# Kernel optimization log

Hardware: AMD Instinct MI355X
Metric: run time of the kernel (lower is better)

## Reference

```python
import jax, jax.numpy as jnp
import numpy as np

U, I, H, E = 50000, 50000, 128, 800000


def segment_softmax(vals, seg, num):
    m = jax.ops.segment_max(vals, seg, num_segments=num)
    ex = jnp.exp(vals - m[seg])
    s = jax.ops.segment_sum(ex, seg, num_segments=num)
    return ex / s[seg]


def setup_inputs() -> dict:
    key = jax.random.key(0)
    ks = jax.random.split(key, 16)
    scale = 1.0 / np.sqrt(H)
    inp = {
        "u_emb": jax.random.normal(ks[0], (U, H), jnp.float32),
        "i_emb": jax.random.normal(ks[1], (I, H), jnp.float32),
        "pVui": jax.random.normal(ks[2], (E, H), jnp.float32),
        "pKiu": jax.random.normal(ks[3], (E, H), jnp.float32),
        "w1": jax.random.normal(ks[4], (H, H), jnp.float32) * scale,
        "w2": jax.random.normal(ks[5], (H, H), jnp.float32) * scale,
        "w1b": jax.random.normal(ks[6], (H, H), jnp.float32) * scale,
        "w2b": jax.random.normal(ks[7], (H, H), jnp.float32) * scale,
        "w3": jax.random.normal(ks[8], (H, H), jnp.float32) * scale,
        "w4": jax.random.normal(ks[9], (H, H), jnp.float32) * scale,
        "edge_index": jax.random.randint(ks[10], (2, E), 0, min(U, I), jnp.int64),
        "last_u": jax.random.randint(ks[11], (2, U), 0, I, jnp.int64),
        "last_i": jax.random.randint(ks[12], (2, I), 0, U, jnp.int64),
        "graph": jnp.zeros((1,), jnp.int64),
    }
    return inp


def reference(u_emb, i_emb, pVui, pKiu, w1, w2, w1b, w2b, w3, w4,
              edge_index, last_u, last_i, graph):
    sqrt_d = np.sqrt(float(u_emb.shape[1])).astype if False else float(np.sqrt(u_emb.shape[1]))
    nu, ni = u_emb.shape[0], i_emb.shape[0]
    src_u, dst_i = edge_index[0], edge_index[1]  # per-edge (user, item)

    # ---- longterm ----
    um_att = u_emb @ w2.T            # [U,H]
    im_att = i_emb @ w1.T            # [I,H]
    # sparse_dense_mul(edge_index, um_att @ im_att.T) -> per-edge dot products
    e_vals = jnp.sum(um_att[src_u] * im_att[dst_i], axis=-1)  # [E]
    e_ui = e_vals + jnp.sum(um_att[src_u] * pVui, axis=-1)
    alphas = segment_softmax(e_ui / sqrt_d, src_u, nu)        # softmax over items per user
    e_iu = e_vals + jnp.sum(im_att[dst_i] * pKiu, axis=-1)
    betas = segment_softmax(e_iu / sqrt_d, dst_i, ni)         # softmax over users per item
    um_b = u_emb @ w2b.T
    im_b = i_emb @ w1b.T
    hLu = jax.ops.segment_sum(alphas[:, None] * (im_b[dst_i] + pKiu), src_u, num_segments=nu)
    hLi = jax.ops.segment_sum(betas[:, None] * (um_b[src_u] + pVui), dst_i, num_segments=ni)

    # ---- shortterm ----
    last_item = i_emb[last_u[1]] @ w3.T   # [U,H] last item embedding per user
    last_user = u_emb[last_i[1]] @ w4.T   # [I,H] last user embedding per item
    a_vals = jnp.sum(last_item[src_u] * im_att[dst_i], axis=-1)
    s_alphas = segment_softmax(a_vals / sqrt_d, src_u, nu)
    b_vals = jnp.sum(last_user[src_u] * im_att[dst_i], axis=-1)
    s_betas = segment_softmax(b_vals / sqrt_d, dst_i, ni)
    # pass_messages with p = ones -> messages + 1
    hSu = jax.ops.segment_sum(s_alphas[:, None] * (im_att[dst_i] + 1.0), src_u, num_segments=nu)
    hSi = jax.ops.segment_sum(s_betas[:, None] * (um_att[src_u] + 1.0), dst_i, num_segments=ni)
    return (hLu, hSu, hLi, hSi)
```

## Files before the change

### kernel.cpp

```cpp
#include <hip/hip_runtime.h>
#include <hip/hip_bf16.h>
#include <math.h>


#define WB 1024

typedef float fvec4 __attribute__((ext_vector_type(4)));

__device__ __forceinline__ float4 nt_load4(const float* p) {
    fvec4 v = __builtin_nontemporal_load((const fvec4*)p);
    return make_float4(v.x, v.y, v.z, v.w);
}
__device__ __forceinline__ float dot4(float4 a, float4 b) {
    return a.x * b.x + a.y * b.y + a.z * b.z + a.w * b.w;
}

struct Gemm6Desc {
    const float* X[6];
    const float* W[6];
    float*       O[6];
    const int*   g[6];
    int          ostride[6];
    int          nrows[6];
};

__global__ __launch_bounds__(256) void gemm6_kernel(Gemm6Desc d)
{
    __shared__ float Xl[64 * 32];
    __shared__ float Wl[128 * 32];
    const int j6 = blockIdx.y;
    const float* __restrict__ X = d.X[j6];
    const float* __restrict__ W = d.W[j6];
    float* __restrict__ O       = d.O[j6];
    const int* __restrict__ gidx = d.g[j6];
    const int ostride = d.ostride[j6];
    const int nrows   = d.nrows[j6];

    const int t  = threadIdx.x;
    const int tx = t & 15;
    const int ty = t >> 4;
    const int brow = blockIdx.x * 64;
    if (brow >= nrows) return;

    float acc[4][8];
#pragma unroll
    for (int j = 0; j < 4; ++j)
#pragma unroll
        for (int i = 0; i < 8; ++i) acc[j][i] = 0.f;

    for (int k0 = 0; k0 < 128; k0 += 32) {
        __syncthreads();
#pragma unroll
        for (int u = 0; u < 2; ++u) {
            int idx4 = t + u * 256;
            int r  = idx4 >> 3;
            int k4 = idx4 & 7;
            int row = brow + r;
            float4 v = make_float4(0.f, 0.f, 0.f, 0.f);
            if (row < nrows) {
                int g = gidx ? gidx[row] : row;
                v = *(const float4*)(X + (size_t)g * 128 + k0 + k4 * 4);
            }
            int sw = k4 ^ ((r >> 3) & 7);
            *(float4*)(Xl + r * 32 + sw * 4) = v;
        }
#pragma unroll
        for (int u = 0; u < 4; ++u) {
            int idx4 = t + u * 256;
            int c  = idx4 >> 3;
            int k4 = idx4 & 7;
            float4 v = *(const float4*)(W + (size_t)c * 128 + k0 + k4 * 4);
            int sw = k4 ^ ((c >> 3) & 7);
            *(float4*)(Wl + c * 32 + sw * 4) = v;
        }
        __syncthreads();
#pragma unroll
        for (int k4 = 0; k4 < 8; ++k4) {
            float4 xv[4], wv[8];
#pragma unroll
            for (int j = 0; j < 4; ++j) {
                int r = ty * 4 + j;
                xv[j] = *(const float4*)(Xl + r * 32 + ((k4 ^ ((r >> 3) & 7)) * 4));
            }
#pragma unroll
            for (int i = 0; i < 8; ++i) {
                int c = tx * 8 + i;
                wv[i] = *(const float4*)(Wl + c * 32 + ((k4 ^ ((c >> 3) & 7)) * 4));
            }
#pragma unroll
            for (int j = 0; j < 4; ++j)
#pragma unroll
                for (int i = 0; i < 8; ++i) {
                    acc[j][i] += xv[j].x * wv[i].x;
                    acc[j][i] += xv[j].y * wv[i].y;
                    acc[j][i] += xv[j].z * wv[i].z;
                    acc[j][i] += xv[j].w * wv[i].w;
                }
        }
    }
#pragma unroll
    for (int j = 0; j < 4; ++j) {
        int row = brow + ty * 4 + j;
        if (row < nrows) {
            float* op = O + (size_t)row * ostride + tx * 8;
            *(float4*)(op)     = make_float4(acc[j][0], acc[j][1], acc[j][2], acc[j][3]);
            *(float4*)(op + 4) = make_float4(acc[j][4], acc[j][5], acc[j][6], acc[j][7]);
        }
    }
}

__global__ __launch_bounds__(256) void hist_kernel(
    const int* __restrict__ ei, int E,
    int* __restrict__ deg_u, int* __restrict__ deg_i)
{
    int e = blockIdx.x * 256 + threadIdx.x;
    if (e < E) {
        atomicAdd(&deg_u[ei[e]], 1);
        atomicAdd(&deg_i[ei[E + e]], 1);
    }
}

__global__ __launch_bounds__(256) void scan_blocksums_kernel(
    const int* __restrict__ deg_u, int nu, int nbu,
    const int* __restrict__ deg_i, int ni,
    int* __restrict__ bsum)
{
    int b = blockIdx.x;
    const int* deg; int n; int base;
    if (b < nbu) { deg = deg_u; n = nu; base = b * WB; }
    else         { deg = deg_i; n = ni; base = (b - nbu) * WB; }
    int t = threadIdx.x;
    int s = 0;
#pragma unroll
    for (int j = 0; j < 4; ++j) {
        int i = base + t * 4 + j;
        if (i < n) s += deg[i];
    }
#pragma unroll
    for (int o = 32; o > 0; o >>= 1) s += __shfl_xor(s, o);
    __shared__ int wt[4];
    if ((t & 63) == 0) wt[t >> 6] = s;
    __syncthreads();
    if (t == 0) bsum[b] = wt[0] + wt[1] + wt[2] + wt[3];
}

__global__ void scan_partials_kernel(
    const int* __restrict__ bsum, int* __restrict__ bscan,
    int nbu, int nbi,
    int* __restrict__ off_u, int nu, int* __restrict__ off_i, int ni)
{
    if (threadIdx.x != 0) return;
    if (blockIdx.x == 0) {
        int c = 0;
        for (int b = 0; b < nbu; ++b) { bscan[b] = c; c += bsum[b]; }
        off_u[nu] = c;
    } else {
        int c = 0;
        for (int b = 0; b < nbi; ++b) { bscan[nbu + b] = c; c += bsum[nbu + b]; }
        off_i[ni] = c;
    }
}

__global__ __launch_bounds__(256) void scan_final_kernel(
    const int* __restrict__ deg_u, int nu, int nbu,
    const int* __restrict__ deg_i, int ni,
    const int* __restrict__ bscan,
    int* __restrict__ off_u, int* __restrict__ cur_u,
    int* __restrict__ off_i, int* __restrict__ cur_i)
{
    int b = blockIdx.x;
    const int* deg; int n; int base; int* off; int* cur;
    if (b < nbu) { deg = deg_u; n = nu; base = b * WB; off = off_u; cur = cur_u; }
    else         { deg = deg_i; n = ni; base = (b - nbu) * WB; off = off_i; cur = cur_i; }
    int t = threadIdx.x;
    int lane = t & 63, w = t >> 6;
    int v[4];
    int s = 0;
#pragma unroll
    for (int j = 0; j < 4; ++j) {
        int i = base + t * 4 + j;
        v[j] = (i < n) ? deg[i] : 0;
        s += v[j];
    }
    int inc = s;
#pragma unroll
    for (int o = 1; o < 64; o <<= 1) {
        int x = __shfl_up(inc, o);
        if (lane >= o) inc += x;
    }
    int excl = inc - s;
    __shared__ int wt[4];
    if (lane == 63) wt[w] = inc;
    __syncthreads();
    int wbase = 0;
    for (int j = 0; j < w; ++j) wbase += wt[j];
    int e = bscan[b] + wbase + excl;
#pragma unroll
    for (int j = 0; j < 4; ++j) {
        int i = base + t * 4 + j;
        if (i < n) { off[i] = e; cur[i] = e; }
        e += v[j];
    }
}

__global__ __launch_bounds__(256) void scatter_ids_kernel(
    const int* __restrict__ ei, int E,
    int* __restrict__ cur_u, int* __restrict__ cur_i,
    int2* __restrict__ eu_list, int2* __restrict__ ei_list)
{
    int e = blockIdx.x * 256 + threadIdx.x;
    if (e < E) {
        int u = ei[e], v = ei[E + e];
        int pu = atomicAdd(&cur_u[u], 1);
        eu_list[pu] = make_int2(v, e);
        int pi = atomicAdd(&cur_i[v], 1);
        ei_list[pi] = make_int2(u, e);
    }
}

__global__ __launch_bounds__(256) void gather_u_kernel(
    const float* __restrict__ fusedU,
    const float* __restrict__ fusedI,
    const float* __restrict__ last_item, const float* __restrict__ last_user,
    const float* __restrict__ pVui, const float* __restrict__ pKiu,
    const int2* __restrict__ lst,
    const int* __restrict__ off_u,
    float2* __restrict__ x24,
    float* __restrict__ hLu, float* __restrict__ hSu, int U, float inv_sqrt_d)
{
    const int wid  = (int)(((size_t)blockIdx.x * blockDim.x + threadIdx.x) >> 6);
    const int lane = threadIdx.x & 63;
    if (wid >= U) return;
    const int g = lane >> 4;
    const int q = lane & 15;

    const float4* fu4 = (const float4*)(fusedU    + (size_t)wid * 256);
    const float4* li4 = (const float4*)(last_item + (size_t)wid * 128);
    const float4* lu4 = (const float4*)(last_user + (size_t)wid * 128);
    const float4 um0 = fu4[q],      um1 = fu4[q + 16];
    const float4 li0 = li4[q],      li1 = li4[q + 16];
    const float4 lu0 = lu4[q],      lu1 = lu4[q + 16];

    float4 a1l = make_float4(0.f,0.f,0.f,0.f), a1h = make_float4(0.f,0.f,0.f,0.f);
    float4 a3l = make_float4(0.f,0.f,0.f,0.f), a3h = make_float4(0.f,0.f,0.f,0.f);
    float s1 = 0.f, s3 = 0.f;
    const int e0 = off_u[wid], e1 = off_u[wid + 1];

    int eA = e0 + g, eB = eA + 4;
    bool vA = eA < e1, vB = eB < e1;
    int2 rA = vA ? lst[eA] : make_int2(0, 0);
    int2 rB = vB ? lst[eB] : rA;

    while (vA) {
        int eA2 = eA + 8, eB2 = eB + 8;
        bool vA2 = eA2 < e1, vB2 = eB2 < e1;
        int2 rA2 = vA2 ? lst[eA2] : make_int2(0, 0);
        int2 rB2 = vB2 ? lst[eB2] : rA2;

        const float4* fIA = (const float4*)(fusedI + (size_t)rA.x * 256);
        const float*  pvA = pVui + (size_t)rA.y * 128;
        const float*  pkA = pKiu + (size_t)rA.y * 128;
        const float4* fIB = (const float4*)(fusedI + (size_t)rB.x * 256);
        const float*  pvB = pVui + (size_t)rB.y * 128;
        const float*  pkB = pKiu + (size_t)rB.y * 128;

        float4 iaA0 = fIA[q],      iaA1 = fIA[q + 16];
        float4 ibA0 = fIA[32 + q], ibA1 = fIA[48 + q];
        float4 pvA0 = nt_load4(pvA + q * 4), pvA1 = nt_load4(pvA + 64 + q * 4);
        float4 pkA0 = nt_load4(pkA + q * 4), pkA1 = nt_load4(pkA + 64 + q * 4);
        float4 iaB0 = fIB[q],      iaB1 = fIB[q + 16];
        float4 ibB0 = fIB[32 + q], ibB1 = fIB[48 + q];
        float4 pvB0 = nt_load4(pvB + q * 4), pvB1 = nt_load4(pvB + 64 + q * 4);
        float4 pkB0 = nt_load4(pkB + q * 4), pkB1 = nt_load4(pkB + 64 + q * 4);

        float pA0 = dot4(um0, iaA0) + dot4(um1, iaA1);
        float qA1 = pA0 + dot4(um0, pvA0) + dot4(um1, pvA1);
        float qA2 = pA0 + dot4(iaA0, pkA0) + dot4(iaA1, pkA1);
        float qA3 = dot4(li0, iaA0) + dot4(li1, iaA1);
        float qA4 = dot4(lu0, iaA0) + dot4(lu1, iaA1);
        float pB0 = dot4(um0, iaB0) + dot4(um1, iaB1);
        float qB1 = pB0 + dot4(um0, pvB0) + dot4(um1, pvB1);
        float qB2 = pB0 + dot4(iaB0, pkB0) + dot4(iaB1, pkB1);
        float qB3 = dot4(li0, iaB0) + dot4(li1, iaB1);
        float qB4 = dot4(lu0, iaB0) + dot4(lu1, iaB1);
#pragma unroll
        for (int o = 8; o > 0; o >>= 1) {
            qA1 += __shfl_xor(qA1, o); qA2 += __shfl_xor(qA2, o);
            qA3 += __shfl_xor(qA3, o); qA4 += __shfl_xor(qA4, o);
            qB1 += __shfl_xor(qB1, o); qB2 += __shfl_xor(qB2, o);
            qB3 += __shfl_xor(qB3, o); qB4 += __shfl_xor(qB4, o);
        }
        float x1A = __expf(qA1 * inv_sqrt_d);
        float x2A = __expf(qA2 * inv_sqrt_d);
        float x3A = __expf(qA3 * inv_sqrt_d);
        float x4A = __expf(qA4 * inv_sqrt_d);
        float mB  = vB ? 1.f : 0.f;
        float x1B = __expf(qB1 * inv_sqrt_d) * mB;
        float x2B = __expf(qB2 * inv_sqrt_d);
        float x3B = __expf(qB3 * inv_sqrt_d) * mB;
        float x4B = __expf(qB4 * inv_sqrt_d);

        a1l.x += x1A*(ibA0.x+pkA0.x) + x1B*(ibB0.x+pkB0.x);
        a1l.y += x1A*(ibA0.y+pkA0.y) + x1B*(ibB0.y+pkB0.y);
        a1l.z += x1A*(ibA0.z+pkA0.z) + x1B*(ibB0.z+pkB0.z);
        a1l.w += x1A*(ibA0.w+pkA0.w) + x1B*(ibB0.w+pkB0.w);
        a1h.x += x1A*(ibA1.x+pkA1.x) + x1B*(ibB1.x+pkB1.x);
        a1h.y += x1A*(ibA1.y+pkA1.y) + x1B*(ibB1.y+pkB1.y);
        a1h.z += x1A*(ibA1.z+pkA1.z) + x1B*(ibB1.z+pkB1.z);
        a1h.w += x1A*(ibA1.w+pkA1.w) + x1B*(ibB1.w+pkB1.w);
        a3l.x += x3A*(iaA0.x+1.f) + x3B*(iaB0.x+1.f);
        a3l.y += x3A*(iaA0.y+1.f) + x3B*(iaB0.y+1.f);
        a3l.z += x3A*(iaA0.z+1.f) + x3B*(iaB0.z+1.f);
        a3l.w += x3A*(iaA0.w+1.f) + x3B*(iaB0.w+1.f);
        a3h.x += x3A*(iaA1.x+1.f) + x3B*(iaB1.x+1.f);
        a3h.y += x3A*(iaA1.y+1.f) + x3B*(iaB1.y+1.f);
        a3h.z += x3A*(iaA1.z+1.f) + x3B*(iaB1.z+1.f);
        a3h.w += x3A*(iaA1.w+1.f) + x3B*(iaB1.w+1.f);
        s1 += x1A + x1B; s3 += x3A + x3B;
        if (q == 0) {
            x24[rA.y] = make_float2(x2A, x4A);
            if (vB) x24[rB.y] = make_float2(x2B, x4B);
        }
        eA = eA2; eB = eB2; vA = vA2; vB = vB2; rA = rA2; rB = rB2;
    }
#pragma unroll
    for (int o = 16; o <= 32; o <<= 1) {
        a1l.x += __shfl_xor(a1l.x, o); a1l.y += __shfl_xor(a1l.y, o);
        a1l.z += __shfl_xor(a1l.z, o); a1l.w += __shfl_xor(a1l.w, o);
        a1h.x += __shfl_xor(a1h.x, o); a1h.y += __shfl_xor(a1h.y, o);
        a1h.z += __shfl_xor(a1h.z, o); a1h.w += __shfl_xor(a1h.w, o);
        a3l.x += __shfl_xor(a3l.x, o); a3l.y += __shfl_xor(a3l.y, o);
        a3l.z += __shfl_xor(a3l.z, o); a3l.w += __shfl_xor(a3l.w, o);
        a3h.x += __shfl_xor(a3h.x, o); a3h.y += __shfl_xor(a3h.y, o);
        a3h.z += __shfl_xor(a3h.z, o); a3h.w += __shfl_xor(a3h.w, o);
        s1 += __shfl_xor(s1, o);       s3 += __shfl_xor(s3, o);
    }
    if (lane < 16) {
        float r1 = (s1 > 0.f) ? 1.f / s1 : 0.f;
        float r3 = (s3 > 0.f) ? 1.f / s3 : 0.f;
        float4* oL = (float4*)(hLu + (size_t)wid * 128);
        float4* oS = (float4*)(hSu + (size_t)wid * 128);
        oL[q]      = make_float4(a1l.x*r1, a1l.y*r1, a1l.z*r1, a1l.w*r1);
        oL[q + 16] = make_float4(a1h.x*r1, a1h.y*r1, a1h.z*r1, a1h.w*r1);
        oS[q]      = make_float4(a3l.x*r3, a3l.y*r3, a3l.z*r3, a3l.w*r3);
        oS[q + 16] = make_float4(a3h.x*r3, a3h.y*r3, a3h.z*r3, a3h.w*r3);
    }
}

__global__ __launch_bounds__(256) void gather_i_kernel(
    const float* __restrict__ fusedU,
    const float* __restrict__ pVui,
    const int2* __restrict__ lst,
    const int* __restrict__ off_i,
    const float2* __restrict__ x24,
    float* __restrict__ hLi, float* __restrict__ hSi, int I)
{
    const int wid  = (int)(((size_t)blockIdx.x * blockDim.x + threadIdx.x) >> 6);
    const int lane = threadIdx.x & 63;
    if (wid >= I) return;
    const int g = lane >> 4;
    const int q = lane & 15;

    float4 a2l = make_float4(0.f,0.f,0.f,0.f), a2h = make_float4(0.f,0.f,0.f,0.f);
    float4 a4l = make_float4(0.f,0.f,0.f,0.f), a4h = make_float4(0.f,0.f,0.f,0.f);
    float s2 = 0.f, s4 = 0.f;
    const int e0 = off_i[wid], e1 = off_i[wid + 1];

    int eA = e0 + g, eB = eA + 4;
    bool vA = eA < e1, vB = eB < e1;
    int2 rA = vA ? lst[eA] : make_int2(0, 0);
    int2 rB = vB ? lst[eB] : rA;

    while (vA) {
        int eA2 = eA + 8, eB2 = eB + 8;
        bool vA2 = eA2 < e1, vB2 = eB2 < e1;
        int2 rA2 = vA2 ? lst[eA2] : make_int2(0, 0);
        int2 rB2 = vB2 ? lst[eB2] : rA2;

        const float4* fUA = (const float4*)(fusedU + (size_t)rA.x * 256);
        const float*  pvA = pVui + (size_t)rA.y * 128;
        const float4* fUB = (const float4*)(fusedU + (size_t)rB.x * 256);
        const float*  pvB = pVui + (size_t)rB.y * 128;

        float2 xA = x24[rA.y];
        float2 xB = x24[rB.y];
        float4 uaA0 = fUA[q],      uaA1 = fUA[q + 16];
        float4 ubA0 = fUA[32 + q], ubA1 = fUA[48 + q];
        float4 pvA0 = nt_load4(pvA + q * 4), pvA1 = nt_load4(pvA + 64 + q * 4);
        float4 uaB0 = fUB[q],      uaB1 = fUB[q + 16];
        float4 ubB0 = fUB[32 + q], ubB1 = fUB[48 + q];
        float4 pvB0 = nt_load4(pvB + q * 4), pvB1 = nt_load4(pvB + 64 + q * 4);

        if (!vB) { xB.x = 0.f; xB.y = 0.f; }
        a2l.x += xA.x*(ubA0.x+pvA0.x) + xB.x*(ubB0.x+pvB0.x);
        a2l.y += xA.x*(ubA0.y+pvA0.y) + xB.x*(ubB0.y+pvB0.y);
        a2l.z += xA.x*(ubA0.z+pvA0.z) + xB.x*(ubB0.z+pvB0.z);
        a2l.w += xA.x*(ubA0.w+pvA0.w) + xB.x*(ubB0.w+pvB0.w);
        a2h.x += xA.x*(ubA1.x+pvA1.x) + xB.x*(ubB1.x+pvB1.x);
        a2h.y += xA.x*(ubA1.y+pvA1.y) + xB.x*(ubB1.y+pvB1.y);
        a2h.z += xA.x*(ubA1.z+pvA1.z) + xB.x*(ubB1.z+pvB1.z);
        a2h.w += xA.x*(ubA1.w+pvA1.w) + xB.x*(ubB1.w+pvB1.w);
        a4l.x += xA.y*(uaA0.x+1.f) + xB.y*(uaB0.x+1.f);
        a4l.y += xA.y*(uaA0.y+1.f) + xB.y*(uaB0.y+1.f);
        a4l.z += xA.y*(uaA0.z+1.f) + xB.y*(uaB0.z+1.f);
        a4l.w += xA.y*(uaA0.w+1.f) + xB.y*(uaB0.w+1.f);
        a4h.x += xA.y*(uaA1.x+1.f) + xB.y*(uaB1.x+1.f);
        a4h.y += xA.y*(uaA1.y+1.f) + xB.y*(uaB1.y+1.f);
        a4h.z += xA.y*(uaA1.z+1.f) + xB.y*(uaB1.z+1.f);
        a4h.w += xA.y*(uaA1.w+1.f) + xB.y*(uaB1.w+1.f);
        s2 += xA.x + xB.x; s4 += xA.y + xB.y;

        eA = eA2; eB = eB2; vA = vA2; vB = vB2; rA = rA2; rB = rB2;
    }
#pragma unroll
    for (int o = 16; o <= 32; o <<= 1) {
        a2l.x += __shfl_xor(a2l.x, o); a2l.y += __shfl_xor(a2l.y, o);
        a2l.z += __shfl_xor(a2l.z, o); a2l.w += __shfl_xor(a2l.w, o);
        a2h.x += __shfl_xor(a2h.x, o); a2h.y += __shfl_xor(a2h.y, o);
        a2h.z += __shfl_xor(a2h.z, o); a2h.w += __shfl_xor(a2h.w, o);
        a4l.x += __shfl_xor(a4l.x, o); a4l.y += __shfl_xor(a4l.y, o);
        a4l.z += __shfl_xor(a4l.z, o); a4l.w += __shfl_xor(a4l.w, o);
        a4h.x += __shfl_xor(a4h.x, o); a4h.y += __shfl_xor(a4h.y, o);
        a4h.z += __shfl_xor(a4h.w - a4h.w + a4h.z, o); a4h.w += __shfl_xor(a4h.w, o);
        s2 += __shfl_xor(s2, o);       s4 += __shfl_xor(s4, o);
    }
    if (lane < 16) {
        float r2 = (s2 > 0.f) ? 1.f / s2 : 0.f;
        float r4 = (s4 > 0.f) ? 1.f / s4 : 0.f;
        float4* oL = (float4*)(hLi + (size_t)wid * 128);
        float4* oS = (float4*)(hSi + (size_t)wid * 128);
        oL[q]      = make_float4(a2l.x*r2, a2l.y*r2, a2l.z*r2, a2l.w*r2);
        oL[q + 16] = make_float4(a2h.x*r2, a2h.y*r2, a2h.z*r2, a2h.w*r2);
        oS[q]      = make_float4(a4l.x*r4, a4l.y*r4, a4l.z*r4, a4l.w*r4);
        oS[q + 16] = make_float4(a4h.x*r4, a4h.y*r4, a4h.z*r4, a4h.w*r4);
    }
}

extern "C" void kernel_launch(void* const* d_in, const int* in_sizes, int n_in,
                              void* d_out, int out_size, void* d_ws, size_t ws_size,
                              hipStream_t stream)
{
    const float* u_emb = (const float*)d_in[0];
    const float* i_emb = (const float*)d_in[1];
    const float* pVui  = (const float*)d_in[2];
    const float* pKiu  = (const float*)d_in[3];
    const float* w1    = (const float*)d_in[4];
    const float* w2    = (const float*)d_in[5];
    const float* w1b   = (const float*)d_in[6];
    const float* w2b   = (const float*)d_in[7];
    const float* w3    = (const float*)d_in[8];
    const float* w4    = (const float*)d_in[9];
    const int* edge_index = (const int*)d_in[10];
    const int* last_u     = (const int*)d_in[11];
    const int* last_i     = (const int*)d_in[12];

    const int U = in_sizes[0] / 128;
    const int I = in_sizes[1] / 128;
    const int E = in_sizes[10] / 2;
    const int nbu = (U + WB - 1) / WB;
    const int nbi = (I + WB - 1) / WB;

    float* ws = (float*)d_ws;
    float* fusedU    = ws;  ws += (size_t)U * 256;
    float* fusedI    = ws;  ws += (size_t)I * 256;
    float* last_item = ws;  ws += (size_t)U * 128;
    float* last_user = ws;  ws += (size_t)I * 128;
    float2* x24 = (float2*)ws;  ws += (size_t)E * 2;
    int2* eu_list = (int2*)ws;  ws += (size_t)E * 2;
    int2* ei_list = (int2*)ws;  ws += (size_t)E * 2;
    int* ip = (int*)ws;
    int* deg_u   = ip;  ip += U;
    int* deg_i   = ip;  ip += I;
    int* off_u   = ip;  ip += U + 1;
    int* off_i   = ip;  ip += I + 1;
    int* cur_u   = ip;  ip += U;
    int* cur_i   = ip;  ip += I;
    int* bsum    = ip;  ip += nbu + nbi;
    int* bscan   = ip;  ip += nbu + nbi;

    float* hLu = (float*)d_out;
    float* hSu = hLu + (size_t)U * 128;
    float* hLi = hSu + (size_t)U * 128;
    float* hSi = hLi + (size_t)I * 128;

    hipMemsetAsync(deg_u, 0, (size_t)(U + I) * sizeof(int), stream);

    dim3 blk(256);
    const int eblk = (E + 255) / 256;
    hist_kernel<<<eblk, blk, 0, stream>>>(edge_index, E, deg_u, deg_i);
    scan_blocksums_kernel<<<nbu + nbi, blk, 0, stream>>>(deg_u, U, nbu, deg_i, I, bsum);
    scan_partials_kernel<<<2, 64, 0, stream>>>(bsum, bscan, nbu, nbi, off_u, U, off_i, I);
    scan_final_kernel<<<nbu + nbi, blk, 0, stream>>>(
        deg_u, U, nbu, deg_i, I, bscan, off_u, cur_u, off_i, cur_i);
    scatter_ids_kernel<<<eblk, blk, 0, stream>>>(edge_index, E, cur_u, cur_i, eu_list, ei_list);

    Gemm6Desc gd;
    gd.X[0] = u_emb; gd.W[0] = w2;  gd.O[0] = fusedU;       gd.g[0] = nullptr;    gd.ostride[0] = 256; gd.nrows[0] = U;
    gd.X[1] = u_emb; gd.W[1] = w2b; gd.O[1] = fusedU + 128; gd.g[1] = nullptr;    gd.ostride[1] = 256; gd.nrows[1] = U;
    gd.X[2] = i_emb; gd.W[2] = w1;  gd.O[2] = fusedI;       gd.g[2] = nullptr;    gd.ostride[2] = 256; gd.nrows[2] = I;
    gd.X[3] = i_emb; gd.W[3] = w1b; gd.O[3] = fusedI + 128; gd.g[3] = nullptr;    gd.ostride[3] = 256; gd.nrows[3] = I;
    gd.X[4] = i_emb; gd.W[4] = w3;  gd.O[4] = last_item;    gd.g[4] = last_u + U; gd.ostride[4] = 128; gd.nrows[4] = U;
    gd.X[5] = u_emb; gd.W[5] = w4;  gd.O[5] = last_user;    gd.g[5] = last_i + I; gd.ostride[5] = 128; gd.nrows[5] = I;
    int maxrows = (U > I) ? U : I;
    dim3 ggrid((maxrows + 63) / 64, 6);
    gemm6_kernel<<<ggrid, blk, 0, stream>>>(gd);

    const float inv_sqrt_d = 1.0f / sqrtf(128.0f);
    gather_u_kernel<<<(U + 3) / 4, blk, 0, stream>>>(
        fusedU, fusedI, last_item, last_user, pVui, pKiu, eu_list,
        off_u, x24, hLu, hSu, U, inv_sqrt_d);
    gather_i_kernel<<<(I + 3) / 4, blk, 0, stream>>>(
        fusedU, pVui, ei_list, off_i, x24, hLi, hSi, I);
}
```

Before: 838.4 us.

## Precompute pVui dot products in edge order and map users to 16-lane groups

Adds a dot_pv kernel that streams pVui once in edge order, computes the user-embedding·pVui dot per edge, and writes it in user-CSR order. This removes the pVui gather from gather_u. gather_u and gather_i now assign one node per 16-lane group instead of one per wavefront, which drops the cross-group shuffle reduction. The per-edge exp weights are written directly into item-CSR positions so gather_i reads them contiguously rather than by edge id. The cost is an extra kernel launch, an upos array and a wider int4 edge list, plus more load imbalance within a wave when node degrees differ.

```diff
diff --git a/kernel.cpp b/kernel.cpp
--- a/kernel.cpp
+++ b/kernel.cpp
@@ -206,37 +206,59 @@
 __global__ __launch_bounds__(256) void scatter_ids_kernel(
     const int* __restrict__ ei, int E,
     int* __restrict__ cur_u, int* __restrict__ cur_i,
-    int2* __restrict__ eu_list, int2* __restrict__ ei_list)
+    int4* __restrict__ eu_list, int2* __restrict__ ei_list,
+    int* __restrict__ upos)
 {
     int e = blockIdx.x * 256 + threadIdx.x;
     if (e < E) {
         int u = ei[e], v = ei[E + e];
         int pu = atomicAdd(&cur_u[u], 1);
-        eu_list[pu] = make_int2(v, e);
         int pi = atomicAdd(&cur_i[v], 1);
+        eu_list[pu] = make_int4(v, e, pi, 0);
         ei_list[pi] = make_int2(u, e);
-    }
+        upos[e] = pu;
+    }
+}
+
+__global__ __launch_bounds__(256) void dot_pv_kernel(
+    const float* __restrict__ fusedU, const float* __restrict__ pVui,
+    const int* __restrict__ ei, const int* __restrict__ upos, int E,
+    float* __restrict__ d1s)
+{
+    const int wav  = (int)(((size_t)blockIdx.x * blockDim.x + threadIdx.x) >> 6);
+    const int lane = threadIdx.x & 63;
+    const int hw = lane >> 5, hl = lane & 31;
+    const int e = wav * 2 + hw;
+    if (e >= E) return;
+    const int src = ei[e];
+    float4 um = ((const float4*)(fusedU + (size_t)src * 256))[hl];
+    float4 pv = nt_load4(pVui + (size_t)e * 128 + hl * 4);
+    float d = dot4(um, pv);
+#pragma unroll
+    for (int o = 16; o > 0; o >>= 1) d += __shfl_xor(d, o);
+    if (hl == 0) d1s[upos[e]] = d;
 }
 
 __global__ __launch_bounds__(256) void gather_u_kernel(
     const float* __restrict__ fusedU,
     const float* __restrict__ fusedI,
     const float* __restrict__ last_item, const float* __restrict__ last_user,
-    const float* __restrict__ pVui, const float* __restrict__ pKiu,
-    const int2* __restrict__ lst,
-    const int* __restrict__ off_u,
-    float2* __restrict__ x24,
+    const float* __restrict__ pKiu,
+    const int4* __restrict__ lst, const int* __restrict__ off_u,
+    const float* __restrict__ d1s,
+    float2* __restrict__ x24s,
     float* __restrict__ hLu, float* __restrict__ hSu, int U, float inv_sqrt_d)
 {
-    const int wid  = (int)(((size_t)blockIdx.x * blockDim.x + threadIdx.x) >> 6);
+    const int wv   = (int)(((size_t)blockIdx.x * blockDim.x + threadIdx.x) >> 6);
     const int lane = threadIdx.x & 63;
-    if (wid >= U) return;
     const int g = lane >> 4;
     const int q = lane & 15;
-
-    const float4* fu4 = (const float4*)(fusedU    + (size_t)wid * 256);
-    const float4* li4 = (const float4*)(last_item + (size_t)wid * 128);
-    const float4* lu4 = (const float4*)(last_user + (size_t)wid * 128);
+    const int uid = wv * 4 + g;
+    if (uid >= U) return;
+
+    const float4* fu4 = (const float4*)(fusedU    + (size_t)uid * 256);
+    const float4* li4 = (const float4*)(last_item + (size_t)uid * 128);
+    const float4* lu4 = (const float4*)(last_user + (size_t)uid * 128);
     const float4 um0 = fu4[q],      um1 = fu4[q + 16];
     const float4 li0 = li4[q],      li1 = li4[q + 16];
     const float4 lu0 = lu4[q],      lu1 = lu4[q + 16];
@@ -244,61 +266,59 @@
     float4 a1l = make_float4(0.f,0.f,0.f,0.f), a1h = make_float4(0.f,0.f,0.f,0.f);
     float4 a3l = make_float4(0.f,0.f,0.f,0.f), a3h = make_float4(0.f,0.f,0.f,0.f);
     float s1 = 0.f, s3 = 0.f;
-    const int e0 = off_u[wid], e1 = off_u[wid + 1];
-
-    int eA = e0 + g, eB = eA + 4;
+    const int e0 = off_u[uid], e1 = off_u[uid + 1];
+
+    int eA = e0, eB = e0 + 1;
     bool vA = eA < e1, vB = eB < e1;
-    int2 rA = vA ? lst[eA] : make_int2(0, 0);
-    int2 rB = vB ? lst[eB] : rA;
+    int4 rA = vA ? lst[eA] : make_int4(0, 0, 0, 0);
+    int4 rB = vB ? lst[eB] : rA;
+    float d1A = vA ? d1s[eA] : 0.f;
+    float d1B = vB ? d1s[eB] : 0.f;
 
     while (vA) {
-        int eA2 = eA + 8, eB2 = eB + 8;
+        int eA2 = eA + 2, eB2 = eB + 2;
         bool vA2 = eA2 < e1, vB2 = eB2 < e1;
-        int2 rA2 = vA2 ? lst[eA2] : make_int2(0, 0);
-        int2 rB2 = vB2 ? lst[eB2] : rA2;
+        int4 rA2 = vA2 ? lst[eA2] : make_int4(0, 0, 0, 0);
+        int4 rB2 = vB2 ? lst[eB2] : rA2;
+        float d1A2 = vA2 ? d1s[eA2] : 0.f;
+        float d1B2 = vB2 ? d1s[eB2] : 0.f;
 
         const float4* fIA = (const float4*)(fusedI + (size_t)rA.x * 256);
-        const float*  pvA = pVui + (size_t)rA.y * 128;
         const float*  pkA = pKiu + (size_t)rA.y * 128;
         const float4* fIB = (const float4*)(fusedI + (size_t)rB.x * 256);
-        const float*  pvB = pVui + (size_t)rB.y * 128;
         const float*  pkB = pKiu + (size_t)rB.y * 128;
 
         float4 iaA0 = fIA[q],      iaA1 = fIA[q + 16];
         float4 ibA0 = fIA[32 + q], ibA1 = fIA[48 + q];
-        float4 pvA0 = nt_load4(pvA + q * 4), pvA1 = nt_load4(pvA + 64 + q * 4);
         float4 pkA0 = nt_load4(pkA + q * 4), pkA1 = nt_load4(pkA + 64 + q * 4);
         float4 iaB0 = fIB[q],      iaB1 = fIB[q + 16];
         float4 ibB0 = fIB[32 + q], ibB1 = fIB[48 + q];
-        float4 pvB0 = nt_load4(pvB + q * 4), pvB1 = nt_load4(pvB + 64 + q * 4);
         float4 pkB0 = nt_load4(pkB + q * 4), pkB1 = nt_load4(pkB + 64 + q * 4);
 
-        float pA0 = dot4(um0, iaA0) + dot4(um1, iaA1);
-        float qA1 = pA0 + dot4(um0, pvA0) + dot4(um1, pvA1);
-        float qA2 = pA0 + dot4(iaA0, pkA0) + dot4(iaA1, pkA1);
-        float qA3 = dot4(li0, iaA0) + dot4(li1, iaA1);
-        float qA4 = dot4(lu0, iaA0) + dot4(lu1, iaA1);
-        float pB0 = dot4(um0, iaB0) + dot4(um1, iaB1);
-        float qB1 = pB0 + dot4(um0, pvB0) + dot4(um1, pvB1);
-        float qB2 = pB0 + dot4(iaB0, pkB0) + dot4(iaB1, pkB1);
-        float qB3 = dot4(li0, iaB0) + dot4(li1, iaB1);
-        float qB4 = dot4(lu0, iaB0) + dot4(lu1, iaB1);
+        float dA0 = dot4(um0, iaA0) + dot4(um1, iaA1);
+        float dA2 = dot4(iaA0, pkA0) + dot4(iaA1, pkA1);
+        float dA3 = dot4(li0, iaA0) + dot4(li1, iaA1);
+        float dA4 = dot4(lu0, iaA0) + dot4(lu1, iaA1);
+        float dB0 = dot4(um0, iaB0) + dot4(um1, iaB1);
+        float dB2 = dot4(iaB0, pkB0) + dot4(iaB1, pkB1);
+        float dB3 = dot4(li0, iaB0) + dot4(li1, iaB1);
+        float dB4 = dot4(lu0, iaB0) + dot4(lu1, iaB1);
 #pragma unroll
         for (int o = 8; o > 0; o >>= 1) {
-            qA1 += __shfl_xor(qA1, o); qA2 += __shfl_xor(qA2, o);
-            qA3 += __shfl_xor(qA3, o); qA4 += __shfl_xor(qA4, o);
-            qB1 += __shfl_xor(qB1, o); qB2 += __shfl_xor(qB2, o);
-            qB3 += __shfl_xor(qB3, o); qB4 += __shfl_xor(qB4, o);
+            dA0 += __shfl_xor(dA0, o); dA2 += __shfl_xor(dA2, o);
+            dA3 += __shfl_xor(dA3, o); dA4 += __shfl_xor(dA4, o);
+            dB0 += __shfl_xor(dB0, o); dB2 += __shfl_xor(dB2, o);
+            dB3 += __shfl_xor(dB3, o); dB4 += __shfl_xor(dB4, o);
         }
-        float x1A = __expf(qA1 * inv_sqrt_d);
-        float x2A = __expf(qA2 * inv_sqrt_d);
-        float x3A = __expf(qA3 * inv_sqrt_d);
-        float x4A = __expf(qA4 * inv_sqrt_d);
+        float x1A = __expf((dA0 + d1A) * inv_sqrt_d);
+        float x2A = __expf((dA0 + dA2) * inv_sqrt_d);
+        float x3A = __expf(dA3 * inv_sqrt_d);
+        float x4A = __expf(dA4 * inv_sqrt_d);
         float mB  = vB ? 1.f : 0.f;
-        float x1B = __expf(qB1 * inv_sqrt_d) * mB;
-        float x2B = __expf(qB2 * inv_sqrt_d);
-        float x3B = __expf(qB3 * inv_sqrt_d) * mB;
-        float x4B = __expf(qB4 * inv_sqrt_d);
+        float x1B = __expf((dB0 + d1B) * inv_sqrt_d) * mB;
+        float x2B = __expf((dB0 + dB2) * inv_sqrt_d);
+        float x3B = __expf(dB3 * inv_sqrt_d) * mB;
+        float x4B = __expf(dB4 * inv_sqrt_d);
 
         a1l.x += x1A*(ibA0.x+pkA0.x) + x1B*(ibB0.x+pkB0.x);
         a1l.y += x1A*(ibA0.y+pkA0.y) + x1B*(ibB0.y+pkB0.y);
@@ -318,72 +338,61 @@
         a3h.w += x3A*(iaA1.w+1.f) + x3B*(iaB1.w+1.f);
         s1 += x1A + x1B; s3 += x3A + x3B;
         if (q == 0) {
-            x24[rA.y] = make_float2(x2A, x4A);
-            if (vB) x24[rB.y] = make_float2(x2B, x4B);
+            x24s[rA.z] = make_float2(x2A, x4A);
+            if (vB) x24s[rB.z] = make_float2(x2B, x4B);
         }
-        eA = eA2; eB = eB2; vA = vA2; vB = vB2; rA = rA2; rB = rB2;
-    }
-#pragma unroll
-    for (int o = 16; o <= 32; o <<= 1) {
-        a1l.x += __shfl_xor(a1l.x, o); a1l.y += __shfl_xor(a1l.y, o);
-        a1l.z += __shfl_xor(a1l.z, o); a1l.w += __shfl_xor(a1l.w, o);
-        a1h.x += __shfl_xor(a1h.x, o); a1h.y += __shfl_xor(a1h.y, o);
-        a1h.z += __shfl_xor(a1h.z, o); a1h.w += __shfl_xor(a1h.w, o);
-        a3l.x += __shfl_xor(a3l.x, o); a3l.y += __shfl_xor(a3l.y, o);
-        a3l.z += __shfl_xor(a3l.z, o); a3l.w += __shfl_xor(a3l.w, o);
-        a3h.x += __shfl_xor(a3h.x, o); a3h.y += __shfl_xor(a3h.y, o);
-        a3h.z += __shfl_xor(a3h.z, o); a3h.w += __shfl_xor(a3h.w, o);
-        s1 += __shfl_xor(s1, o);       s3 += __shfl_xor(s3, o);
-    }
-    if (lane < 16) {
-        float r1 = (s1 > 0.f) ? 1.f / s1 : 0.f;
-        float r3 = (s3 > 0.f) ? 1.f / s3 : 0.f;
-        float4* oL = (float4*)(hLu + (size_t)wid * 128);
-        float4* oS = (float4*)(hSu + (size_t)wid * 128);
-        oL[q]      = make_float4(a1l.x*r1, a1l.y*r1, a1l.z*r1, a1l.w*r1);
-        oL[q + 16] = make_float4(a1h.x*r1, a1h.y*r1, a1h.z*r1, a1h.w*r1);
-        oS[q]      = make_float4(a3l.x*r3, a3l.y*r3, a3l.z*r3, a3l.w*r3);
-        oS[q + 16] = make_float4(a3h.x*r3, a3h.y*r3, a3h.z*r3, a3h.w*r3);
-    }
+        eA = eA2; eB = eB2; vA = vA2; vB = vB2;
+        rA = rA2; rB = rB2; d1A = d1A2; d1B = d1B2;
+    }
+    float r1 = (s1 > 0.f) ? 1.f / s1 : 0.f;
+    float r3 = (s3 > 0.f) ? 1.f / s3 : 0.f;
+    float4* oL = (float4*)(hLu + (size_t)uid * 128);
+    float4* oS = (float4*)(hSu + (size_t)uid * 128);
+    oL[q]      = make_float4(a1l.x*r1, a1l.y*r1, a1l.z*r1, a1l.w*r1);
+    oL[q + 16] = make_float4(a1h.x*r1, a1h.y*r1, a1h.z*r1, a1h.w*r1);
+    oS[q]      = make_float4(a3l.x*r3, a3l.y*r3, a3l.z*r3, a3l.w*r3);
+    oS[q + 16] = make_float4(a3h.x*r3, a3h.y*r3, a3h.z*r3, a3h.w*r3);
 }
 
 __global__ __launch_bounds__(256) void gather_i_kernel(
     const float* __restrict__ fusedU,
     const float* __restrict__ pVui,
-    const int2* __restrict__ lst,
-    const int* __restrict__ off_i,
-    const float2* __restrict__ x24,
+    const int2* __restrict__ lst, const int* __restrict__ off_i,
+    const float2* __restrict__ x24s,
     float* __restrict__ hLi, float* __restrict__ hSi, int I)
 {
-    const int wid  = (int)(((size_t)blockIdx.x * blockDim.x + threadIdx.x) >> 6);
+    const int wv   = (int)(((size_t)blockIdx.x * blockDim.x + threadIdx.x) >> 6);
     const int lane = threadIdx.x & 63;
-    if (wid >= I) return;
     const int g = lane >> 4;
     const int q = lane & 15;
+    const int iid = wv * 4 + g;
+    if (iid >= I) return;
 
     float4 a2l = make_float4(0.f,0.f,0.f,0.f), a2h = make_float4(0.f,0.f,0.f,0.f);
     float4 a4l = make_float4(0.f,0.f,0.f,0.f), a4h = make_float4(0.f,0.f,0.f,0.f);
     float s2 = 0.f, s4 = 0.f;
-    const int e0 = off_i[wid], e1 = off_i[wid + 1];
-
-    int eA = e0 + g, eB = eA + 4;
+    const int e0 = off_i[iid], e1 = off_i[iid + 1];
+
+    int eA = e0, eB = e0 + 1;
     bool vA = eA < e1, vB = eB < e1;
     int2 rA = vA ? lst[eA] : make_int2(0, 0);
     int2 rB = vB ? lst[eB] : rA;
+    float2 xA = vA ? x24s[eA] : make_float2(0.f, 0.f);
+    float2 xB = vB ? x24s[eB] : make_float2(0.f, 0.f);
 
     while (vA) {
-        int eA2 = eA + 8, eB2 = eB + 8;
+        int eA2 = eA + 2, eB2 = eB + 2;
         bool vA2 = eA2 < e1, vB2 = eB2 < e1;
         int2 rA2 = vA2 ? lst[eA2] : make_int2(0, 0);
         int2 rB2 = vB2 ? lst[eB2] : rA2;
+        float2 xA2v = vA2 ? x24s[eA2] : make_float2(0.f, 0.f);
+        float2 xB2v = vB2 ? x24s[eB2] : make_float2(0.f, 0.f);
 
         const float4* fUA = (const float4*)(fusedU + (size_t)rA.x * 256);
         const float*  pvA = pVui + (size_t)rA.y * 128;
         const float4* fUB = (const float4*)(fusedU + (size_t)rB.x * 256);
         const float*  pvB = pVui + (size_t)rB.y * 128;
 
-        float2 xA = x24[rA.y];
-        float2 xB = x24[rB.y];
         float4 uaA0 = fUA[q],      uaA1 = fUA[q + 16];
         float4 ubA0 = fUA[32 + q], ubA1 = fUA[48 + q];
         float4 pvA0 = nt_load4(pvA + q * 4), pvA1 = nt_load4(pvA + 64 + q * 4);
@@ -391,7 +400,6 @@
         float4 ubB0 = fUB[32 + q], ubB1 = fUB[48 + q];
         float4 pvB0 = nt_load4(pvB + q * 4), pvB1 = nt_load4(pvB + 64 + q * 4);
 
-        if (!vB) { xB.x = 0.f; xB.y = 0.f; }
         a2l.x += xA.x*(ubA0.x+pvA0.x) + xB.x*(ubB0.x+pvB0.x);
         a2l.y += xA.x*(ubA0.y+pvA0.y) + xB.x*(ubB0.y+pvB0.y);
         a2l.z += xA.x*(ubA0.z+pvA0.z) + xB.x*(ubB0.z+pvB0.z);
@@ -410,30 +418,17 @@
         a4h.w += xA.y*(uaA1.w+1.f) + xB.y*(uaB1.w+1.f);
         s2 += xA.x + xB.x; s4 += xA.y + xB.y;
 
-        eA = eA2; eB = eB2; vA = vA2; vB = vB2; rA = rA2; rB = rB2;
-    }
-#pragma unroll
-    for (int o = 16; o <= 32; o <<= 1) {
-        a2l.x += __shfl_xor(a2l.x, o); a2l.y += __shfl_xor(a2l.y, o);
-        a2l.z += __shfl_xor(a2l.z, o); a2l.w += __shfl_xor(a2l.w, o);
-        a2h.x += __shfl_xor(a2h.x, o); a2h.y += __shfl_xor(a2h.y, o);
-        a2h.z += __shfl_xor(a2h.z, o); a2h.w += __shfl_xor(a2h.w, o);
-        a4l.x += __shfl_xor(a4l.x, o); a4l.y += __shfl_xor(a4l.y, o);
-        a4l.z += __shfl_xor(a4l.z, o); a4l.w += __shfl_xor(a4l.w, o);
-        a4h.x += __shfl_xor(a4h.x, o); a4h.y += __shfl_xor(a4h.y, o);
-        a4h.z += __shfl_xor(a4h.w - a4h.w + a4h.z, o); a4h.w += __shfl_xor(a4h.w, o);
-        s2 += __shfl_xor(s2, o);       s4 += __shfl_xor(s4, o);
-    }
-    if (lane < 16) {
-        float r2 = (s2 > 0.f) ? 1.f / s2 : 0.f;
-        float r4 = (s4 > 0.f) ? 1.f / s4 : 0.f;
-        float4* oL = (float4*)(hLi + (size_t)wid * 128);
-        float4* oS = (float4*)(hSi + (size_t)wid * 128);
-        oL[q]      = make_float4(a2l.x*r2, a2l.y*r2, a2l.z*r2, a2l.w*r2);
-        oL[q + 16] = make_float4(a2h.x*r2, a2h.y*r2, a2h.z*r2, a2h.w*r2);
-        oS[q]      = make_float4(a4l.x*r4, a4l.y*r4, a4l.z*r4, a4l.w*r4);
-        oS[q + 16] = make_float4(a4h.x*r4, a4h.y*r4, a4h.z*r4, a4h.w*r4);
-    }
+        eA = eA2; eB = eB2; vA = vA2; vB = vB2;
+        rA = rA2; rB = rB2; xA = xA2v; xB = xB2v;
+    }
+    float r2 = (s2 > 0.f) ? 1.f / s2 : 0.f;
+    float r4 = (s4 > 0.f) ? 1.f / s4 : 0.f;
+    float4* oL = (float4*)(hLi + (size_t)iid * 128);
+    float4* oS = (float4*)(hSi + (size_t)iid * 128);
+    oL[q]      = make_float4(a2l.x*r2, a2l.y*r2, a2l.z*r2, a2l.w*r2);
+    oL[q + 16] = make_float4(a2h.x*r2, a2h.y*r2, a2h.z*r2, a2h.w*r2);
+    oS[q]      = make_float4(a4l.x*r4, a4l.y*r4, a4l.z*r4, a4l.w*r4);
+    oS[q + 16] = make_float4(a4h.x*r4, a4h.y*r4, a4h.z*r4, a4h.w*r4);
 }
 
 extern "C" void kernel_launch(void* const* d_in, const int* in_sizes, int n_in,
@@ -465,10 +460,12 @@
     float* fusedI    = ws;  ws += (size_t)I * 256;
     float* last_item = ws;  ws += (size_t)U * 128;
     float* last_user = ws;  ws += (size_t)I * 128;
-    float2* x24 = (float2*)ws;  ws += (size_t)E * 2;
-    int2* eu_list = (int2*)ws;  ws += (size_t)E * 2;
+    float* d1s = ws;            ws += E;
+    float2* x24s = (float2*)ws; ws += (size_t)E * 2;
+    int4* eu_list = (int4*)ws;  ws += (size_t)E * 4;
     int2* ei_list = (int2*)ws;  ws += (size_t)E * 2;
     int* ip = (int*)ws;
+    int* upos    = ip;  ip += E;
     int* deg_u   = ip;  ip += U;
     int* deg_i   = ip;  ip += I;
     int* off_u   = ip;  ip += U + 1;
@@ -492,7 +489,8 @@
     scan_partials_kernel<<<2, 64, 0, stream>>>(bsum, bscan, nbu, nbi, off_u, U, off_i, I);
     scan_final_kernel<<<nbu + nbi, blk, 0, stream>>>(
         deg_u, U, nbu, deg_i, I, bscan, off_u, cur_u, off_i, cur_i);
-    scatter_ids_kernel<<<eblk, blk, 0, stream>>>(edge_index, E, cur_u, cur_i, eu_list, ei_list);
+    scatter_ids_kernel<<<eblk, blk, 0, stream>>>(
+        edge_index, E, cur_u, cur_i, eu_list, ei_list, upos);
 
     Gemm6Desc gd;
     gd.X[0] = u_emb; gd.W[0] = w2;  gd.O[0] = fusedU;       gd.g[0] = nullptr;    gd.ostride[0] = 256; gd.nrows[0] = U;
@@ -506,9 +504,11 @@
     gemm6_kernel<<<ggrid, blk, 0, stream>>>(gd);
 
     const float inv_sqrt_d = 1.0f / sqrtf(128.0f);
-    gather_u_kernel<<<(U + 3) / 4, blk, 0, stream>>>(
-        fusedU, fusedI, last_item, last_user, pVui, pKiu, eu_list,
-        off_u, x24, hLu, hSu, U, inv_sqrt_d);
-    gather_i_kernel<<<(I + 3) / 4, blk, 0, stream>>>(
-        fusedU, pVui, ei_list, off_i, x24, hLi, hSi, I);
-}
+    dot_pv_kernel<<<(E + 7) / 8, blk, 0, stream>>>(
+        fusedU, pVui, edge_index, upos, E, d1s);
+    gather_u_kernel<<<(U + 15) / 16, blk, 0, stream>>>(
+        fusedU, fusedI, last_item, last_user, pKiu, eu_list, off_u, d1s,
+        x24s, hLu, hSu, U, inv_sqrt_d);
+    gather_i_kernel<<<(I + 15) / 16, blk, 0, stream>>>(
+        fusedU, pVui, ei_list, off_i, x24s, hLi, hSi, I);
+}
```

Measured after the change: 960.0 us. +14.5%, slower.
